# Optimization experiments

Measured on AMD Instinct MI355X. Metric: run time of the kernel, lower is better.

The kernel has to match this reference:

```python
import jax, jax.numpy as jnp
import numpy as np

N = 50000   # nodes of the target node type
E = 800000  # edges per incoming edge type (avg degree 16)
D = 128     # in == hidden == out channels (required by the module's pooling layer)


def sage_mean(x, edge_index, Wl, bl, Wr):
    """PyG SAGEConv with mean aggregation: lin_l(mean_j x_j) + lin_r(x_i).
    Note: per the original code, sources are gathered from the TARGET node
    feature table (x_input = x_dict[tgt_node_type])."""
    src, tgt = edge_index[0], edge_index[1]
    msg = x[src]                                                   # [E, D] gather
    agg = jax.ops.segment_sum(msg, tgt, num_segments=x.shape[0])   # [N, D] scatter-add
    cnt = jax.ops.segment_sum(jnp.ones((edge_index.shape[1],), x.dtype), tgt,
                              num_segments=x.shape[0])             # [N] degree
    agg = agg / jnp.maximum(cnt, 1.0)[:, None]                     # mean; 0 for isolated nodes
    return agg @ Wl + bl + x @ Wr                                  # [N, D]


def setup_inputs() -> dict:
    key = jax.random.key(0)
    ks = jax.random.split(key, 6)
    s = 1.0 / np.sqrt(D)
    x = jax.random.normal(ks[0], (N, D), jnp.float32)
    edge_index_a = jax.random.randint(ks[1], (2, E), 0, N)
    edge_index_b = jax.random.randint(ks[2], (2, E), 0, N)
    Wl = jax.random.normal(ks[3], (D, D), jnp.float32) * s
    Wr = jax.random.normal(ks[4], (D, D), jnp.float32) * s
    bl = jnp.zeros((D,), jnp.float32)
    Wp = jax.random.normal(ks[5], (D, D), jnp.float32) * s
    bp = jnp.zeros((D,), jnp.float32)
    return {"x": x, "Wl": Wl, "bl": bl, "Wr": Wr, "Wp": Wp, "bp": bp,
            "edge_index_a": edge_index_a, "edge_index_b": edge_index_b}


def reference(x, Wl, bl, Wr, Wp, bp, edge_index_a, edge_index_b):
    # One SAGEConv encoder + pooling Linear shared across incoming edge types,
    # softmax per edge type, then mean over edge types (torch.stack(...).mean(0)).
    outs = []
    for ei in (edge_index_a, edge_index_b):
        h = sage_mean(x, ei, Wl, bl, Wr)            # [N, D]
        outs.append(jax.nn.softmax(h @ Wp + bp, axis=-1))
    return (outs[0] + outs[1]) * 0.5                # [N, D]
```

## Files before the change

### kernel.cpp

```cpp
#include <hip/hip_runtime.h>
#include <math.h>

constexpr int D    = 128;
constexpr int BT   = 128;
constexpr int TILE = 4096;

using bf16x8 = __attribute__((ext_vector_type(8))) short;
using f32x4  = __attribute__((ext_vector_type(4))) float;
#define MFMA16 __builtin_amdgcn_mfma_f32_16x16x32_bf16

__device__ __forceinline__ unsigned short f2bf(float f) {
    unsigned u = __builtin_bit_cast(unsigned, f);
    u = (u + 0x7FFF + ((u >> 16) & 1)) >> 16;
    return (unsigned short)u;
}

__global__ __launch_bounds__(256)
void convert_kernel(const float* __restrict__ x, unsigned short* __restrict__ x_bf,
                    int total4)
{
    for (int i = blockIdx.x * 256 + threadIdx.x; i < total4;
         i += gridDim.x * 256) {
        float4 v = reinterpret_cast<const float4*>(x)[i];
        ushort4 o;
        o.x = f2bf(v.x); o.y = f2bf(v.y); o.z = f2bf(v.z); o.w = f2bf(v.w);
        reinterpret_cast<ushort4*>(x_bf)[i] = o;
    }
}

__global__ __launch_bounds__(256)
void bucket_kernel(const int* __restrict__ ea, int Ea,
                   const int* __restrict__ eb, int Eb,
                   unsigned int* __restrict__ ent_a, int* __restrict__ cnt_a,
                   unsigned int* __restrict__ ent_b, int* __restrict__ cnt_b,
                   int NBKT, int CAP, int GA)
{
    __shared__ int hist[512];
    __shared__ int base[512];

    const int bid  = blockIdx.x;
    const int type = (bid >= GA);
    const int* e   = type ? eb : ea;
    const int  E   = type ? Eb : Ea;
    unsigned int* ent = type ? ent_b : ent_a;
    int* cnt          = type ? cnt_b : cnt_a;

    const int t  = threadIdx.x;
    const int i0 = (bid - type * GA) * TILE;

    for (int h = t; h < NBKT; h += 256) hist[h] = 0;
    __syncthreads();

    int tgts[16];
    #pragma unroll
    for (int j = 0; j < 16; ++j) {
        int i = i0 + j * 256 + t;
        tgts[j] = (i < E) ? e[(size_t)E + i] : -1;
        if (tgts[j] >= 0) atomicAdd(&hist[tgts[j] >> 7], 1);
    }
    __syncthreads();

    for (int h = t; h < NBKT; h += 256) {
        base[h] = (hist[h] > 0) ? atomicAdd(&cnt[h], hist[h]) : 0;
        hist[h] = 0;
    }
    __syncthreads();

    #pragma unroll
    for (int j = 0; j < 16; ++j) {
        int i = i0 + j * 256 + t;
        if (tgts[j] >= 0) {
            int b   = tgts[j] >> 7;
            int pos = base[b] + atomicAdd(&hist[b], 1);
            int src = e[i];
            if (pos < CAP)
                ent[(size_t)b * CAP + pos] = ((unsigned)src << 7) | (tgts[j] & 127);
        }
    }
}

__global__ __launch_bounds__(512)
void agg_bucket_kernel(const unsigned short* __restrict__ x_bf,
                       const unsigned int* __restrict__ ent_a, const int* __restrict__ cnt_a,
                       const unsigned int* __restrict__ ent_b, const int* __restrict__ cnt_b,
                       unsigned short* __restrict__ mean_a, unsigned short* __restrict__ mean_b,
                       int N, int NBKT, int CAP)
{
    extern __shared__ __align__(16) char smem_raw[];
    int* tmp  = (int*)smem_raw;
    int* off  = tmp + CAP;
    int* cur  = off + BT + 1;
    int* wtot = cur + BT;
    unsigned short* srcl = (unsigned short*)(wtot + 2);

    const int bid  = blockIdx.x;
    const int type = (bid >= NBKT);
    const int k    = bid - type * NBKT;
    const unsigned int* ent = type ? ent_b : ent_a;
    unsigned short* mean    = type ? mean_b : mean_a;
    const int cnt = min((type ? cnt_b : cnt_a)[k], CAP);

    const int t = threadIdx.x, l = t & 63, w = t >> 6;

    if (t < BT) off[t] = 0;
    __syncthreads();

    for (int i = t; i < cnt; i += 512) {
        unsigned e = ent[(size_t)k * CAP + i];
        tmp[i] = (int)e;
        atomicAdd(&off[e & (BT - 1)], 1);
    }
    __syncthreads();

    int v = 0, s = 0;
    if (t < BT) {
        v = off[t]; s = v;
        #pragma unroll
        for (int o = 1; o < 64; o <<= 1) {
            int u = __shfl_up(s, o, 64);
            if (l >= o) s += u;
        }
        if (l == 63) wtot[w] = s;
    }
    __syncthreads();
    if (t < BT) {
        int ex = ((w == 1) ? wtot[0] : 0) + s - v;
        off[t] = ex; cur[t] = ex;
    }
    if (t == 0) off[BT] = wtot[0] + wtot[1];
    __syncthreads();

    for (int i = t; i < cnt; i += 512) {
        unsigned e = (unsigned)tmp[i];
        int pos = atomicAdd(&cur[e & (BT - 1)], 1);
        srcl[pos] = (unsigned short)(e >> 7);
    }
    __syncthreads();

    const int node0 = k * BT;
    for (int tt = w; tt < BT; tt += 8) {
        int n = node0 + tt;
        if (n >= N) break;
        int o0 = off[tt], o1 = off[tt + 1];
        float ax = 0.f, ay = 0.f;
        int j = o0;
        for (; j + 4 <= o1; j += 4) {
            int s0 = srcl[j], s1 = srcl[j + 1], s2 = srcl[j + 2], s3 = srcl[j + 3];
            unsigned v0 = *(const unsigned*)(x_bf + (size_t)s0 * D + 2 * l);
            unsigned v1 = *(const unsigned*)(x_bf + (size_t)s1 * D + 2 * l);
            unsigned v2 = *(const unsigned*)(x_bf + (size_t)s2 * D + 2 * l);
            unsigned v3 = *(const unsigned*)(x_bf + (size_t)s3 * D + 2 * l);
            ax += __builtin_bit_cast(float, v0 << 16) + __builtin_bit_cast(float, v1 << 16)
                + __builtin_bit_cast(float, v2 << 16) + __builtin_bit_cast(float, v3 << 16);
            ay += __builtin_bit_cast(float, v0 & 0xffff0000u) + __builtin_bit_cast(float, v1 & 0xffff0000u)
                + __builtin_bit_cast(float, v2 & 0xffff0000u) + __builtin_bit_cast(float, v3 & 0xffff0000u);
        }
        for (; j < o1; ++j) {
            int ss = srcl[j];
            unsigned vv = *(const unsigned*)(x_bf + (size_t)ss * D + 2 * l);
            ax += __builtin_bit_cast(float, vv << 16);
            ay += __builtin_bit_cast(float, vv & 0xffff0000u);
        }
        float r = 1.0f / fmaxf((float)(o1 - o0), 1.0f);
        unsigned o = ((unsigned)f2bf(ay * r) << 16) | f2bf(ax * r);
        *(unsigned*)(mean + (size_t)n * D + 2 * l) = o;
    }
}

__global__ __launch_bounds__(256)
void repack_kernel(const float* __restrict__ Wl, const float* __restrict__ Wr,
                   const float* __restrict__ Wp,
                   unsigned short* __restrict__ WlB, unsigned short* __restrict__ WrB,
                   unsigned short* __restrict__ WpB)
{
    int gw = (blockIdx.x * 256 + threadIdx.x) >> 6;
    int l  = threadIdx.x & 63;
    const float* W = (gw < 32) ? Wl : (gw < 64) ? Wr : Wp;
    unsigned short* O = (gw < 32) ? WlB : (gw < 64) ? WrB : WpB;
    int ktnt = gw & 31, kt = ktnt >> 3, nt = ktnt & 7;
    bf16x8 v;
    #pragma unroll
    for (int j = 0; j < 8; ++j)
        v[j] = (short)f2bf(W[(size_t)(kt * 32 + (l >> 4) * 8 + j) * D + nt * 16 + (l & 15)]);
    *reinterpret_cast<bf16x8*>(O + ((size_t)ktnt * 64 + l) * 8) = v;
}

__global__ __launch_bounds__(256)
void gemm_kernel(const unsigned short* __restrict__ mean_a,
                 const unsigned short* __restrict__ mean_b,
                 const unsigned short* __restrict__ x_bf,
                 const unsigned short* __restrict__ WlB,
                 const unsigned short* __restrict__ WrB,
                 const unsigned short* __restrict__ WpB,
                 const float* __restrict__ bl, const float* __restrict__ bp,
                 float* __restrict__ out, int N)
{
    __shared__ unsigned short hA[64 * D];
    __shared__ unsigned short hB[64 * D];

    const int t = threadIdx.x, w = t >> 6, l = t & 63;
    const int q = l & 15;
    const int kg = l >> 4;
    const int node0 = blockIdx.x * 64 + w * 16;
    const int arow = min(node0 + q, N - 1);

    bf16x8 fa[4], fb[4], fx[4];
    #pragma unroll
    for (int kt = 0; kt < 4; ++kt) {
        size_t o = (size_t)arow * D + kt * 32 + kg * 8;
        fa[kt] = *reinterpret_cast<const bf16x8*>(mean_a + o);
        fb[kt] = *reinterpret_cast<const bf16x8*>(mean_b + o);
        fx[kt] = *reinterpret_cast<const bf16x8*>(x_bf + o);
    }

    #pragma unroll
    for (int nt = 0; nt < 8; ++nt) {
        f32x4 ca = {0.f, 0.f, 0.f, 0.f};
        f32x4 cb = {0.f, 0.f, 0.f, 0.f};
        #pragma unroll
        for (int kt = 0; kt < 4; ++kt) {
            const size_t fo = ((size_t)(kt * 8 + nt) * 64 + l) * 8;
            bf16x8 wl = *reinterpret_cast<const bf16x8*>(WlB + fo);
            bf16x8 wr = *reinterpret_cast<const bf16x8*>(WrB + fo);
            ca = MFMA16(fa[kt], wl, ca, 0, 0, 0);
            ca = MFMA16(fx[kt], wr, ca, 0, 0, 0);
            cb = MFMA16(fb[kt], wl, cb, 0, 0, 0);
            cb = MFMA16(fx[kt], wr, cb, 0, 0, 0);
        }
        float blv = bl[nt * 16 + q];
        #pragma unroll
        for (int r = 0; r < 4; ++r) {
            int lrow = w * 16 + kg * 4 + r;
            int byte = lrow * 256 + (nt * 16 + q) * 2;
            byte ^= ((lrow & 7) << 4);
            *reinterpret_cast<unsigned short*>(reinterpret_cast<char*>(hA) + byte) = f2bf(ca[r] + blv);
            *reinterpret_cast<unsigned short*>(reinterpret_cast<char*>(hB) + byte) = f2bf(cb[r] + blv);
        }
    }
    __syncthreads();

    bf16x8 ga[4], gb[4];
    #pragma unroll
    for (int kt = 0; kt < 4; ++kt) {
        int lrow = w * 16 + q;
        int byte = lrow * 256 + kt * 64 + kg * 16;
        byte ^= ((lrow & 7) << 4);
        ga[kt] = *reinterpret_cast<bf16x8*>(reinterpret_cast<char*>(hA) + byte);
        gb[kt] = *reinterpret_cast<bf16x8*>(reinterpret_cast<char*>(hB) + byte);
    }

    f32x4 la[8], lb[8];
    #pragma unroll
    for (int nt = 0; nt < 8; ++nt) {
        la[nt] = f32x4{0.f, 0.f, 0.f, 0.f};
        lb[nt] = f32x4{0.f, 0.f, 0.f, 0.f};
        #pragma unroll
        for (int kt = 0; kt < 4; ++kt) {
            const size_t fo = ((size_t)(kt * 8 + nt) * 64 + l) * 8;
            bf16x8 wp = *reinterpret_cast<const bf16x8*>(WpB + fo);
            la[nt] = MFMA16(ga[kt], wp, la[nt], 0, 0, 0);
            lb[nt] = MFMA16(gb[kt], wp, lb[nt], 0, 0, 0);
        }
        float bpv = bp[nt * 16 + q];
        #pragma unroll
        for (int r = 0; r < 4; ++r) { la[nt][r] += bpv; lb[nt][r] += bpv; }
    }

    #pragma unroll
    for (int r = 0; r < 4; ++r) {
        float ma = -INFINITY, mb = -INFINITY;
        #pragma unroll
        for (int nt = 0; nt < 8; ++nt) {
            ma = fmaxf(ma, la[nt][r]);
            mb = fmaxf(mb, lb[nt][r]);
        }
        #pragma unroll
        for (int o = 1; o < 16; o <<= 1) {
            ma = fmaxf(ma, __shfl_xor(ma, o, 64));
            mb = fmaxf(mb, __shfl_xor(mb, o, 64));
        }
        float ea[8], eb[8], sa = 0.f, sb = 0.f;
        #pragma unroll
        for (int nt = 0; nt < 8; ++nt) {
            ea[nt] = __expf(la[nt][r] - ma); sa += ea[nt];
            eb[nt] = __expf(lb[nt][r] - mb); sb += eb[nt];
        }
        #pragma unroll
        for (int o = 1; o < 16; o <<= 1) {
            sa += __shfl_xor(sa, o, 64);
            sb += __shfl_xor(sb, o, 64);
        }
        float ra = 0.5f / sa, rb = 0.5f / sb;
        int grow = node0 + kg * 4 + r;
        if (grow < N) {
            float* o = out + (size_t)grow * D + q;
            #pragma unroll
            for (int nt = 0; nt < 8; ++nt)
                o[nt * 16] = ea[nt] * ra + eb[nt] * rb;
        }
    }
}

extern "C" void kernel_launch(void* const* d_in, const int* in_sizes, int n_in,
                              void* d_out, int out_size, void* d_ws, size_t ws_size,
                              hipStream_t stream)
{
    const float* x  = (const float*)d_in[0];
    const float* Wl = (const float*)d_in[1];
    const float* bl = (const float*)d_in[2];
    const float* Wr = (const float*)d_in[3];
    const float* Wp = (const float*)d_in[4];
    const float* bp = (const float*)d_in[5];
    const int*   ea = (const int*)d_in[6];
    const int*   eb = (const int*)d_in[7];

    const int N  = in_sizes[0] / D;
    const int Ea = in_sizes[6] / 2;
    const int Eb = in_sizes[7] / 2;

    const int NBKT = (N + BT - 1) / BT;
    const int Emax = Ea > Eb ? Ea : Eb;
    const int CAP  = (int)(((long long)Emax * BT / N) * 5 / 4 + 128);

    unsigned int* ent_a = (unsigned int*)d_ws;
    unsigned int* ent_b = ent_a + (size_t)NBKT * CAP;
    int* cnt_a = (int*)(ent_b + (size_t)NBKT * CAP);
    int* cnt_b = cnt_a + NBKT;
    uintptr_t p = (uintptr_t)(cnt_b + NBKT);
    p = (p + 15) & ~(uintptr_t)15;
    unsigned short* mean_a = (unsigned short*)p;
    unsigned short* mean_b = mean_a + (size_t)N * D;
    unsigned short* x_bf   = mean_b + (size_t)N * D;
    unsigned short* WlB    = x_bf + (size_t)N * D;
    unsigned short* WrB    = WlB + D * D;
    unsigned short* WpB    = WrB + D * D;

    hipMemsetAsync(cnt_a, 0, sizeof(int) * 2 * (size_t)NBKT, stream);

    convert_kernel<<<1024, 256, 0, stream>>>(x, x_bf, N * D / 4);

    const int GA = (Ea + TILE - 1) / TILE;
    const int GB = (Eb + TILE - 1) / TILE;
    bucket_kernel<<<GA + GB, 256, 0, stream>>>(ea, Ea, eb, Eb,
                                               ent_a, cnt_a, ent_b, cnt_b,
                                               NBKT, CAP, GA);

    repack_kernel<<<24, 256, 0, stream>>>(Wl, Wr, Wp, WlB, WrB, WpB);

    const int smem = CAP * 6 + (BT + 1 + BT + 2) * 4 + 16;
    agg_bucket_kernel<<<2 * NBKT, 512, smem, stream>>>(
        x_bf, ent_a, cnt_a, ent_b, cnt_b, mean_a, mean_b, N, NBKT, CAP);

    gemm_kernel<<<(N + 63) / 64, 256, 0, stream>>>(
        mean_a, mean_b, x_bf, WlB, WrB, WpB, bl, bp, (float*)d_out, N);
}
```

Measured before the change: 149.7 us.

## Slice feature table into 32-column planes and split sort from gather

Stores the bf16 feature table and the mean outputs as four 32-column planes of 64 bytes per row. The gather is split into its own kernel that runs one block per (bucket, slice), so each block's working set of source rows is smaller and more cache friendly. Per-bucket sorting of edges now writes its compacted source lists and offsets to global memory for the gather kernel to read. Convert, bucket and weight repack are merged into a single launch. The split adds extra global traffic for the sorted lists and four times as many gather blocks, each reloading those lists.

After: 150.7 us. Within noise of the previous version (+0.7%).

```diff
diff --git a/kernel.cpp b/kernel.cpp
--- a/kernel.cpp
+++ b/kernel.cpp
@@ -16,75 +16,89 @@
 }
 
 __global__ __launch_bounds__(256)
-void convert_kernel(const float* __restrict__ x, unsigned short* __restrict__ x_bf,
-                    int total4)
-{
-    for (int i = blockIdx.x * 256 + threadIdx.x; i < total4;
-         i += gridDim.x * 256) {
-        float4 v = reinterpret_cast<const float4*>(x)[i];
-        ushort4 o;
-        o.x = f2bf(v.x); o.y = f2bf(v.y); o.z = f2bf(v.z); o.w = f2bf(v.w);
-        reinterpret_cast<ushort4*>(x_bf)[i] = o;
-    }
-}
-
-__global__ __launch_bounds__(256)
-void bucket_kernel(const int* __restrict__ ea, int Ea,
-                   const int* __restrict__ eb, int Eb,
-                   unsigned int* __restrict__ ent_a, int* __restrict__ cnt_a,
-                   unsigned int* __restrict__ ent_b, int* __restrict__ cnt_b,
-                   int NBKT, int CAP, int GA)
+void prep_kernel(const float* __restrict__ x, unsigned short* __restrict__ x_bfs,
+                 const int* __restrict__ ea, int Ea,
+                 const int* __restrict__ eb, int Eb,
+                 unsigned int* __restrict__ ent_a, int* __restrict__ cnt_a,
+                 unsigned int* __restrict__ ent_b, int* __restrict__ cnt_b,
+                 const float* __restrict__ Wl, const float* __restrict__ Wr,
+                 const float* __restrict__ Wp,
+                 unsigned short* __restrict__ WlB, unsigned short* __restrict__ WrB,
+                 unsigned short* __restrict__ WpB,
+                 int N, int NBKT, int CAP, int GA, int GB, int GCONV)
 {
     __shared__ int hist[512];
     __shared__ int base[512];
 
-    const int bid  = blockIdx.x;
-    const int type = (bid >= GA);
-    const int* e   = type ? eb : ea;
-    const int  E   = type ? Eb : Ea;
-    unsigned int* ent = type ? ent_b : ent_a;
-    int* cnt          = type ? cnt_b : cnt_a;
-
-    const int t  = threadIdx.x;
-    const int i0 = (bid - type * GA) * TILE;
-
-    for (int h = t; h < NBKT; h += 256) hist[h] = 0;
-    __syncthreads();
-
-    int tgts[16];
-    #pragma unroll
-    for (int j = 0; j < 16; ++j) {
-        int i = i0 + j * 256 + t;
-        tgts[j] = (i < E) ? e[(size_t)E + i] : -1;
-        if (tgts[j] >= 0) atomicAdd(&hist[tgts[j] >> 7], 1);
-    }
-    __syncthreads();
-
-    for (int h = t; h < NBKT; h += 256) {
-        base[h] = (hist[h] > 0) ? atomicAdd(&cnt[h], hist[h]) : 0;
-        hist[h] = 0;
-    }
-    __syncthreads();
-
-    #pragma unroll
-    for (int j = 0; j < 16; ++j) {
-        int i = i0 + j * 256 + t;
-        if (tgts[j] >= 0) {
-            int b   = tgts[j] >> 7;
-            int pos = base[b] + atomicAdd(&hist[b], 1);
-            int src = e[i];
-            if (pos < CAP)
-                ent[(size_t)b * CAP + pos] = ((unsigned)src << 7) | (tgts[j] & 127);
-        }
+    const int bid = blockIdx.x;
+    const int t   = threadIdx.x;
+
+    if (bid < GA + GB) {
+        const int type = (bid >= GA);
+        const int* e   = type ? eb : ea;
+        const int  E   = type ? Eb : Ea;
+        unsigned int* ent = type ? ent_b : ent_a;
+        int* cnt          = type ? cnt_b : cnt_a;
+        const int i0 = (bid - type * GA) * TILE;
+
+        for (int h = t; h < NBKT; h += 256) hist[h] = 0;
+        __syncthreads();
+
+        int tgts[16];
+        #pragma unroll
+        for (int j = 0; j < 16; ++j) {
+            int i = i0 + j * 256 + t;
+            tgts[j] = (i < E) ? e[(size_t)E + i] : -1;
+            if (tgts[j] >= 0) atomicAdd(&hist[tgts[j] >> 7], 1);
+        }
+        __syncthreads();
+
+        for (int h = t; h < NBKT; h += 256) {
+            base[h] = (hist[h] > 0) ? atomicAdd(&cnt[h], hist[h]) : 0;
+            hist[h] = 0;
+        }
+        __syncthreads();
+
+        #pragma unroll
+        for (int j = 0; j < 16; ++j) {
+            int i = i0 + j * 256 + t;
+            if (tgts[j] >= 0) {
+                int b   = tgts[j] >> 7;
+                int pos = base[b] + atomicAdd(&hist[b], 1);
+                if (pos < CAP)
+                    ent[(size_t)b * CAP + pos] = ((unsigned)e[i] << 7) | (tgts[j] & 127);
+            }
+        }
+    } else if (bid < GA + GB + GCONV) {
+        const int total4 = N * 32;
+        for (int i = (bid - GA - GB) * 256 + t; i < total4; i += GCONV * 256) {
+            int n  = i >> 5;
+            int j4 = i & 31;
+            float4 v = reinterpret_cast<const float4*>(x)[i];
+            ushort4 o;
+            o.x = f2bf(v.x); o.y = f2bf(v.y); o.z = f2bf(v.z); o.w = f2bf(v.w);
+            int s = j4 >> 3, c = (j4 & 7) * 4;
+            *reinterpret_cast<ushort4*>(x_bfs + ((size_t)s * N + n) * 32 + c) = o;
+        }
+    } else {
+        int gw = ((bid - GA - GB - GCONV) * 256 + t) >> 6;
+        int l  = t & 63;
+        const float* W = (gw < 32) ? Wl : (gw < 64) ? Wr : Wp;
+        unsigned short* O = (gw < 32) ? WlB : (gw < 64) ? WrB : WpB;
+        int ktnt = gw & 31, kt = ktnt >> 3, nt = ktnt & 7;
+        bf16x8 v;
+        #pragma unroll
+        for (int j = 0; j < 8; ++j)
+            v[j] = (short)f2bf(W[(size_t)(kt * 32 + (l >> 4) * 8 + j) * D + nt * 16 + (l & 15)]);
+        *reinterpret_cast<bf16x8*>(O + ((size_t)ktnt * 64 + l) * 8) = v;
     }
 }
 
 __global__ __launch_bounds__(512)
-void agg_bucket_kernel(const unsigned short* __restrict__ x_bf,
-                       const unsigned int* __restrict__ ent_a, const int* __restrict__ cnt_a,
-                       const unsigned int* __restrict__ ent_b, const int* __restrict__ cnt_b,
-                       unsigned short* __restrict__ mean_a, unsigned short* __restrict__ mean_b,
-                       int N, int NBKT, int CAP)
+void sort_kernel(const unsigned int* __restrict__ ent_a, const int* __restrict__ cnt_a,
+                 const unsigned int* __restrict__ ent_b, const int* __restrict__ cnt_b,
+                 unsigned short* __restrict__ srcl_g, int* __restrict__ off_g,
+                 int NBKT, int CAP)
 {
     extern __shared__ __align__(16) char smem_raw[];
     int* tmp  = (int*)smem_raw;
@@ -97,7 +111,6 @@
     const int type = (bid >= NBKT);
     const int k    = bid - type * NBKT;
     const unsigned int* ent = type ? ent_b : ent_a;
-    unsigned short* mean    = type ? mean_b : mean_a;
     const int cnt = min((type ? cnt_b : cnt_a)[k], CAP);
 
     const int t = threadIdx.x, l = t & 63, w = t >> 6;
@@ -137,58 +150,81 @@
     }
     __syncthreads();
 
-    const int node0 = k * BT;
-    for (int tt = w; tt < BT; tt += 8) {
-        int n = node0 + tt;
+    for (int i = t; i < cnt; i += 512)
+        srcl_g[(size_t)bid * CAP + i] = srcl[i];
+    if (t <= BT)
+        off_g[(size_t)bid * (BT + 1) + t] = off[t];
+}
+
+__global__ __launch_bounds__(256)
+void gather_kernel(const unsigned short* __restrict__ x_bfs,
+                   const unsigned short* __restrict__ srcl_g,
+                   const int* __restrict__ off_g,
+                   unsigned short* __restrict__ mean_a_s,
+                   unsigned short* __restrict__ mean_b_s,
+                   int N, int NBKT, int CAP)
+{
+    extern __shared__ __align__(16) char smem_raw[];
+    int* off = (int*)smem_raw;
+    unsigned short* srcl = (unsigned short*)(off + BT + 1);
+
+    const int bid   = blockIdx.x;
+    const int slice = bid & 3;
+    const int tb    = bid >> 2;
+    const int type  = (tb >= NBKT);
+    const int k     = tb - type * NBKT;
+
+    const int t = threadIdx.x, l = t & 63, w = t >> 6;
+    const int q = l >> 4, c = l & 15;
+
+    const int cnt = off_g[(size_t)tb * (BT + 1) + BT];
+    for (int i = t; i <= BT; i += 256)
+        off[i] = off_g[(size_t)tb * (BT + 1) + i];
+    for (int i = t; i < cnt; i += 256)
+        srcl[i] = srcl_g[(size_t)tb * CAP + i];
+    __syncthreads();
+
+    const unsigned short* xs = x_bfs + (size_t)slice * N * 32;
+    unsigned short* mean = (type ? mean_b_s : mean_a_s) + (size_t)slice * N * 32;
+
+    for (int tt = w; tt < BT; tt += 4) {
+        const int n = k * BT + tt;
         if (n >= N) break;
-        int o0 = off[tt], o1 = off[tt + 1];
+        const int o0 = off[tt], o1 = off[tt + 1];
         float ax = 0.f, ay = 0.f;
-        int j = o0;
-        for (; j + 4 <= o1; j += 4) {
-            int s0 = srcl[j], s1 = srcl[j + 1], s2 = srcl[j + 2], s3 = srcl[j + 3];
-            unsigned v0 = *(const unsigned*)(x_bf + (size_t)s0 * D + 2 * l);
-            unsigned v1 = *(const unsigned*)(x_bf + (size_t)s1 * D + 2 * l);
-            unsigned v2 = *(const unsigned*)(x_bf + (size_t)s2 * D + 2 * l);
-            unsigned v3 = *(const unsigned*)(x_bf + (size_t)s3 * D + 2 * l);
-            ax += __builtin_bit_cast(float, v0 << 16) + __builtin_bit_cast(float, v1 << 16)
-                + __builtin_bit_cast(float, v2 << 16) + __builtin_bit_cast(float, v3 << 16);
-            ay += __builtin_bit_cast(float, v0 & 0xffff0000u) + __builtin_bit_cast(float, v1 & 0xffff0000u)
-                + __builtin_bit_cast(float, v2 & 0xffff0000u) + __builtin_bit_cast(float, v3 & 0xffff0000u);
-        }
-        for (; j < o1; ++j) {
-            int ss = srcl[j];
-            unsigned vv = *(const unsigned*)(x_bf + (size_t)ss * D + 2 * l);
-            ax += __builtin_bit_cast(float, vv << 16);
-            ay += __builtin_bit_cast(float, vv & 0xffff0000u);
-        }
+
+        int j = o0 + q;
+        for (; j + 4 < o1; j += 8) {
+            int s0 = srcl[j], s1 = srcl[j + 4];
+            unsigned v0 = *(const unsigned*)(xs + (size_t)s0 * 32 + c * 2);
+            unsigned v1 = *(const unsigned*)(xs + (size_t)s1 * 32 + c * 2);
+            ax += __builtin_bit_cast(float, v0 << 16)
+                + __builtin_bit_cast(float, v1 << 16);
+            ay += __builtin_bit_cast(float, v0 & 0xffff0000u)
+                + __builtin_bit_cast(float, v1 & 0xffff0000u);
+        }
+        if (j < o1) {
+            int s0 = srcl[j];
+            unsigned v0 = *(const unsigned*)(xs + (size_t)s0 * 32 + c * 2);
+            ax += __builtin_bit_cast(float, v0 << 16);
+            ay += __builtin_bit_cast(float, v0 & 0xffff0000u);
+        }
+
+        ax += __shfl_xor(ax, 16, 64); ax += __shfl_xor(ax, 32, 64);
+        ay += __shfl_xor(ay, 16, 64); ay += __shfl_xor(ay, 32, 64);
+
         float r = 1.0f / fmaxf((float)(o1 - o0), 1.0f);
-        unsigned o = ((unsigned)f2bf(ay * r) << 16) | f2bf(ax * r);
-        *(unsigned*)(mean + (size_t)n * D + 2 * l) = o;
+        if (q == 0) {
+            unsigned o = ((unsigned)f2bf(ay * r) << 16) | f2bf(ax * r);
+            *(unsigned*)(mean + (size_t)n * 32 + c * 2) = o;
+        }
     }
 }
 
 __global__ __launch_bounds__(256)
-void repack_kernel(const float* __restrict__ Wl, const float* __restrict__ Wr,
-                   const float* __restrict__ Wp,
-                   unsigned short* __restrict__ WlB, unsigned short* __restrict__ WrB,
-                   unsigned short* __restrict__ WpB)
-{
-    int gw = (blockIdx.x * 256 + threadIdx.x) >> 6;
-    int l  = threadIdx.x & 63;
-    const float* W = (gw < 32) ? Wl : (gw < 64) ? Wr : Wp;
-    unsigned short* O = (gw < 32) ? WlB : (gw < 64) ? WrB : WpB;
-    int ktnt = gw & 31, kt = ktnt >> 3, nt = ktnt & 7;
-    bf16x8 v;
-    #pragma unroll
-    for (int j = 0; j < 8; ++j)
-        v[j] = (short)f2bf(W[(size_t)(kt * 32 + (l >> 4) * 8 + j) * D + nt * 16 + (l & 15)]);
-    *reinterpret_cast<bf16x8*>(O + ((size_t)ktnt * 64 + l) * 8) = v;
-}
-
-__global__ __launch_bounds__(256)
-void gemm_kernel(const unsigned short* __restrict__ mean_a,
-                 const unsigned short* __restrict__ mean_b,
-                 const unsigned short* __restrict__ x_bf,
+void gemm_kernel(const unsigned short* __restrict__ mean_a_s,
+                 const unsigned short* __restrict__ mean_b_s,
+                 const unsigned short* __restrict__ x_bfs,
                  const unsigned short* __restrict__ WlB,
                  const unsigned short* __restrict__ WrB,
                  const unsigned short* __restrict__ WpB,
@@ -207,10 +243,10 @@
     bf16x8 fa[4], fb[4], fx[4];
     #pragma unroll
     for (int kt = 0; kt < 4; ++kt) {
-        size_t o = (size_t)arow * D + kt * 32 + kg * 8;
-        fa[kt] = *reinterpret_cast<const bf16x8*>(mean_a + o);
-        fb[kt] = *reinterpret_cast<const bf16x8*>(mean_b + o);
-        fx[kt] = *reinterpret_cast<const bf16x8*>(x_bf + o);
+        size_t o = ((size_t)kt * N + arow) * 32 + kg * 8;
+        fa[kt] = *reinterpret_cast<const bf16x8*>(mean_a_s + o);
+        fb[kt] = *reinterpret_cast<const bf16x8*>(mean_b_s + o);
+        fx[kt] = *reinterpret_cast<const bf16x8*>(x_bfs + o);
     }
 
     #pragma unroll
@@ -320,37 +356,41 @@
 
     const int NBKT = (N + BT - 1) / BT;
     const int Emax = Ea > Eb ? Ea : Eb;
-    const int CAP  = (int)(((long long)Emax * BT / N) * 5 / 4 + 128);
+    int CAP = (int)(((long long)Emax * BT / N) * 5 / 4 + 128);
+    CAP = (CAP + 7) & ~7;
 
     unsigned int* ent_a = (unsigned int*)d_ws;
     unsigned int* ent_b = ent_a + (size_t)NBKT * CAP;
     int* cnt_a = (int*)(ent_b + (size_t)NBKT * CAP);
     int* cnt_b = cnt_a + NBKT;
-    uintptr_t p = (uintptr_t)(cnt_b + NBKT);
+    int* off_g = cnt_b + NBKT;
+    uintptr_t p = (uintptr_t)(off_g + (size_t)2 * NBKT * (BT + 1));
     p = (p + 15) & ~(uintptr_t)15;
-    unsigned short* mean_a = (unsigned short*)p;
-    unsigned short* mean_b = mean_a + (size_t)N * D;
-    unsigned short* x_bf   = mean_b + (size_t)N * D;
-    unsigned short* WlB    = x_bf + (size_t)N * D;
-    unsigned short* WrB    = WlB + D * D;
-    unsigned short* WpB    = WrB + D * D;
+    unsigned short* srcl_g  = (unsigned short*)p;
+    unsigned short* x_bfs   = srcl_g + (size_t)2 * NBKT * CAP;
+    unsigned short* mean_a_s = x_bfs + (size_t)N * D;
+    unsigned short* mean_b_s = mean_a_s + (size_t)N * D;
+    unsigned short* WlB     = mean_b_s + (size_t)N * D;
+    unsigned short* WrB     = WlB + D * D;
+    unsigned short* WpB     = WrB + D * D;
 
     hipMemsetAsync(cnt_a, 0, sizeof(int) * 2 * (size_t)NBKT, stream);
-
-    convert_kernel<<<1024, 256, 0, stream>>>(x, x_bf, N * D / 4);
 
     const int GA = (Ea + TILE - 1) / TILE;
     const int GB = (Eb + TILE - 1) / TILE;
-    bucket_kernel<<<GA + GB, 256, 0, stream>>>(ea, Ea, eb, Eb,
-                                               ent_a, cnt_a, ent_b, cnt_b,
-                                               NBKT, CAP, GA);
-
-    repack_kernel<<<24, 256, 0, stream>>>(Wl, Wr, Wp, WlB, WrB, WpB);
-
-    const int smem = CAP * 6 + (BT + 1 + BT + 2) * 4 + 16;
-    agg_bucket_kernel<<<2 * NBKT, 512, smem, stream>>>(
-        x_bf, ent_a, cnt_a, ent_b, cnt_b, mean_a, mean_b, N, NBKT, CAP);
+    const int GCONV = 512;
+    prep_kernel<<<GA + GB + GCONV + 24, 256, 0, stream>>>(
+        x, x_bfs, ea, Ea, eb, Eb, ent_a, cnt_a, ent_b, cnt_b,
+        Wl, Wr, Wp, WlB, WrB, WpB, N, NBKT, CAP, GA, GB, GCONV);
+
+    const int smem_sort = CAP * 6 + (BT + 1 + BT + 2) * 4 + 16;
+    sort_kernel<<<2 * NBKT, 512, smem_sort, stream>>>(
+        ent_a, cnt_a, ent_b, cnt_b, srcl_g, off_g, NBKT, CAP);
+
+    const int smem_gather = (BT + 1) * 4 + CAP * 2 + 16;
+    gather_kernel<<<8 * NBKT, 256, smem_gather, stream>>>(
+        x_bfs, srcl_g, off_g, mean_a_s, mean_b_s, N, NBKT, CAP);
 
     gemm_kernel<<<(N + 63) / 64, 256, 0, stream>>>(
-        mean_a, mean_b, x_bf, WlB, WrB, WpB, bl, bp, (float*)d_out, N);
-}
+        mean_a_s, mean_b_s, x_bfs, WlB, WrB, WpB, bl, bp, (float*)d_out, N);
+}
```
